# Kernel optimization log

Measured on AMD Instinct MI355X. Metric: run time of the kernel, lower is better.

## Reference

```python
import jax, jax.numpy as jnp
import numpy as np

B, T, DIM, HEADS, DH = 4, 2048, 1024, 16, 64  # dh = dim // heads


def setup_inputs() -> dict:
    key = jax.random.key(0)
    k1, k2, k3 = jax.random.split(key, 3)
    x = jax.random.normal(k1, (B, T, DIM), dtype=jnp.float32)
    # nn.Linear weights, stored as [in, out] for x @ W convention
    W_qkv = jax.random.normal(k2, (DIM, 3 * HEADS * DH), dtype=jnp.float32) * (DIM ** -0.5)
    W_o = jax.random.normal(k3, (HEADS * DH, DIM), dtype=jnp.float32) * ((HEADS * DH) ** -0.5)
    return {"x": x, "W_qkv": W_qkv, "W_o": W_o}


def reference(x, W_qkv, W_o):
    b, t, _ = x.shape
    qkv = x @ W_qkv  # [b, t, 3*h*dh]
    # einops 'b t (d k h) -> k b h t d' with k=3, h=HEADS: fused axis splits as (dh, 3, h)
    qkv = qkv.reshape(b, t, DH, 3, HEADS)
    qkv = jnp.transpose(qkv, (3, 0, 4, 1, 2))  # [3, b, h, t, dh]
    q, k, v = qkv[0], qkv[1], qkv[2]
    scale = DH ** -0.5
    scores = jnp.einsum('bhid,bhjd->bhij', q, k) * scale  # [b, h, t, t]
    attn = jax.nn.softmax(scores, axis=-1)
    out = jnp.einsum('bhij,bhjd->bhid', attn, v)  # [b, h, t, dh]
    out = jnp.transpose(out, (0, 2, 1, 3)).reshape(b, t, HEADS * DH)  # 'b h t d -> b t (h d)'
    return out @ W_o
```

## Files before the change

kernel.cpp:

```cpp
#include <hip/hip_runtime.h>

typedef __bf16 bf16;
typedef __bf16 bf16x2 __attribute__((ext_vector_type(2)));
typedef __bf16 bf16x4 __attribute__((ext_vector_type(4)));
typedef __bf16 bf16x8 __attribute__((ext_vector_type(8)));
typedef float  f32x4  __attribute__((ext_vector_type(4)));
typedef float  f32x16 __attribute__((ext_vector_type(16)));
typedef unsigned int u32;
typedef unsigned int u32x2 __attribute__((ext_vector_type(2)));
typedef unsigned int u32x4 __attribute__((ext_vector_type(4)));

#define LOG2E 1.44269504088896340736f
#define EXP_SC (0.125f * LOG2E)

#if __has_builtin(__builtin_amdgcn_exp2f)
#define EXP2F(x) __builtin_amdgcn_exp2f(x)
#else
#define EXP2F(x) __builtin_exp2f(x)
#endif

__device__ __forceinline__ u32 pk_bf16(float lo, float hi) {
  u32 a = __float_as_uint(lo) + 0x8000u;
  u32 b = __float_as_uint(hi) + 0x8000u;
  return __builtin_amdgcn_perm(b, a, 0x07060302);
}
#if __has_builtin(__builtin_amdgcn_cvt_pk_bf16_f32)
__device__ __forceinline__ u32 cvtpk(float lo, float hi) {
  bf16x2 t = __builtin_amdgcn_cvt_pk_bf16_f32(lo, hi);
  return __builtin_bit_cast(u32, t);
}
#else
__device__ __forceinline__ u32 cvtpk(float lo, float hi) { return pk_bf16(lo, hi); }
#endif
__device__ __forceinline__ unsigned short bf16r(float x) {
  return (unsigned short)((__float_as_uint(x) + 0x8000u) >> 16);
}

__device__ __forceinline__ f32x16 zero16() {
  f32x16 a;
#pragma unroll
  for (int i = 0; i < 16; i++) a[i] = 0.f;
  return a;
}

__device__ __forceinline__ void async_ld16(void* lds, const void* g) {
  __builtin_amdgcn_global_load_lds(
      (const __attribute__((address_space(1))) void*)(g),
      (__attribute__((address_space(3))) void*)(lds),
      16, 0, 0);
}

__global__ void prep_all(const float* __restrict__ x,    bf16* __restrict__ xb,
                         const float* __restrict__ Wqkv, bf16* __restrict__ wqkvT,
                         const float* __restrict__ Wo,   bf16* __restrict__ woT) {
  __shared__ float s[12288];
  const int bid = blockIdx.x;
  const int tid = threadIdx.x;
  if (bid < 8192) {
    int i = bid * 256 + tid;
    float4 v = ((const float4*)x)[i];
    u32x2 o = { pk_bf16(v.x, v.y), pk_bf16(v.z, v.w) };
    *(u32x2*)(xb + (size_t)i * 4) = o;
  } else if (bid < 8448) {
    const int k0 = (bid - 8192) * 4;
    for (int i = tid; i < 3072; i += 256) {
      int r = i / 768, c = (i - r * 768) * 4;
      *(float4*)(s + r * 3072 + c) = *(const float4*)(Wqkv + (size_t)(k0 + r) * 3072 + c);
    }
    __syncthreads();
    for (int n = tid; n < 3072; n += 256) {
      int dl = n & 63, h = (n >> 6) & 15, wch = n >> 10;
      int d = ((dl & 15) << 2) | (dl >> 4);
      int on = d * 48 + wch * 16 + h;
      u32x2 v = { pk_bf16(s[0 * 3072 + on], s[1 * 3072 + on]),
                  pk_bf16(s[2 * 3072 + on], s[3 * 3072 + on]) };
      *(u32x2*)(wqkvT + (size_t)n * 1024 + k0) = v;
    }
  } else {
    const int k0 = (bid - 8448) * 8;
    for (int i = tid; i < 2048; i += 256) {
      int r = i >> 8, c = (i & 255) * 4;
      *(float4*)(s + r * 1024 + c) = *(const float4*)(Wo + (size_t)(k0 + r) * 1024 + c);
    }
    __syncthreads();
    for (int n = tid; n < 1024; n += 256) {
      u32x4 v = { pk_bf16(s[0 * 1024 + n], s[1 * 1024 + n]),
                  pk_bf16(s[2 * 1024 + n], s[3 * 1024 + n]),
                  pk_bf16(s[4 * 1024 + n], s[5 * 1024 + n]),
                  pk_bf16(s[6 * 1024 + n], s[7 * 1024 + n]) };
      *(u32x4*)(woT + (size_t)n * 1024 + k0) = v;
    }
  }
}

template <int MODE>
__launch_bounds__(256, 2)
__global__ void gemm_bt(const bf16* __restrict__ A, const bf16* __restrict__ BT,
                        float* __restrict__ C, int N,
                        bf16* __restrict__ Qb, bf16* __restrict__ Kb, bf16* __restrict__ Vb) {
  constexpr int K = 1024;
  __shared__ bf16 sA[128 * 64];
  __shared__ bf16 sB[128 * 64];
  const int m0 = blockIdx.x * 128;
  const int n0 = blockIdx.y * 128;
  const int tid = threadIdx.x;
  const int lane = tid & 63;
  const int w = tid >> 6;
  const int wm = (w >> 1) * 64, wn = (w & 1) * 64;
  const int l15 = lane & 15, quad = lane >> 4;

  f32x4 acc[4][4];
  for (int i = 0; i < 4; i++)
    for (int j = 0; j < 4; j++) acc[i][j] = f32x4{0.f, 0.f, 0.f, 0.f};

  const int rT = tid >> 3;
  const int jT = (tid & 7) ^ (rT & 7);
  const bf16* gA = A  + (size_t)(m0 + rT) * K + jT * 8;
  const bf16* gB = BT + (size_t)(n0 + rT) * K + jT * 8;

  for (int k0 = 0; k0 < K; k0 += 64) {
    __syncthreads();
    for (int i = 0; i < 4; i++) {
      async_ld16((void*)(sA + (i * 256 + w * 64) * 8), gA + (size_t)i * 32 * K);
      async_ld16((void*)(sB + (i * 256 + w * 64) * 8), gB + (size_t)i * 32 * K);
    }
    gA += 64; gB += 64;
    __syncthreads();

    for (int kk = 0; kk < 2; kk++) {
      bf16x8 af[4], bfr[4];
      for (int ms = 0; ms < 4; ms++) {
        int r = wm + ms * 16 + l15;
        af[ms] = *(const bf16x8*)(sA + r * 64 + (((kk * 4 + quad) ^ (r & 7)) * 8));
      }
      for (int ns = 0; ns < 4; ns++) {
        int r = wn + ns * 16 + l15;
        bfr[ns] = *(const bf16x8*)(sB + r * 64 + (((kk * 4 + quad) ^ (r & 7)) * 8));
      }
      for (int ms = 0; ms < 4; ms++)
        for (int ns = 0; ns < 4; ns++)
          acc[ms][ns] = __builtin_amdgcn_mfma_f32_16x16x32_bf16(af[ms], bfr[ns], acc[ms][ns], 0, 0, 0);
    }
  }

  if (MODE == 0) {
    for (int ms = 0; ms < 4; ms++)
      for (int ns = 0; ns < 4; ns++)
        for (int r = 0; r < 4; r++) {
          int row = m0 + wm + ms * 16 + quad * 4 + r;
          int col = n0 + wn + ns * 16 + l15;
          C[(size_t)row * N + col] = acc[ms][ns][r];
        }
  } else {
    const int col0 = n0 + wn;
    const int wch = col0 >> 10;
    const int h = (col0 >> 6) & 15;
    if (wch != 2) {
      bf16* dst = (wch == 0) ? Qb : Kb;
      const float sc = (wch == 0) ? EXP_SC : 1.0f;
      for (int ms = 0; ms < 4; ms++)
        for (int r = 0; r < 4; r++) {
          int row = m0 + wm + ms * 16 + quad * 4 + r;
          int b = row >> 11, t = row & 2047;
          u32x2 v = { cvtpk(acc[ms][0][r] * sc, acc[ms][1][r] * sc),
                      cvtpk(acc[ms][2][r] * sc, acc[ms][3][r] * sc) };
          *(u32x2*)((unsigned short*)dst +
                    (((size_t)(b * 16 + h)) * 2048 + t) * 64 + l15 * 4) = v;
        }
    } else {
      for (int ms = 0; ms < 4; ms++)
        for (int ns = 0; ns < 4; ns++) {
          int row = m0 + wm + ms * 16 + quad * 4;
          int b = row >> 11, t = row & 2047;
          int d = l15 * 4 + ns;
          u32x2 v = { cvtpk(acc[ms][ns][0], acc[ms][ns][1]),
                      cvtpk(acc[ms][ns][2], acc[ms][ns][3]) };
          *(u32x2*)((unsigned short*)Vb +
                    (((size_t)(b * 16 + h)) * 64 + d) * 2048 + t) = v;
        }
    }
  }
}

__launch_bounds__(256, 3)
__global__ void attn_fwd(const bf16* __restrict__ Q, const bf16* __restrict__ K,
                         const bf16* __restrict__ VT, bf16* __restrict__ O) {
  __shared__ bf16 sK[64 * 64];
  __shared__ bf16 sV[4][64 * 64];
  const int bh = blockIdx.x;
  const int q0 = blockIdx.y * 128;
  const int tid = threadIdx.x;
  const int lane = tid & 63, w = tid >> 6;
  const int l31 = lane & 31, hi = lane >> 5;

  bf16x8 qf[4];
  {
    const bf16* qp = Q + ((size_t)bh * 2048 + q0 + w * 32 + l31) * 64 + hi * 8;
#pragma unroll
    for (int kq = 0; kq < 4; kq++) qf[kq] = *(const bf16x8*)(qp + kq * 16);
  }

  f32x16 oacc[2];
  oacc[0] = zero16(); oacc[1] = zero16();
  float rs = 0.f;

  const int cA = w * 128 + lane;
  const int rA = cA >> 3, jA = (cA & 7) ^ (rA & 7);
  const bf16* gK = K  + ((size_t)bh * 2048 + rA) * 64 + jA * 8;
  const bf16* gV = VT + ((size_t)bh * 64 + rA) * 2048 + jA * 8;

  int fo[2][4];
#pragma unroll
  for (int sub = 0; sub < 2; sub++)
#pragma unroll
    for (int st = 0; st < 4; st++) {
      int r = sub * 32 + l31;
      fo[sub][st] = r * 64 + (((st * 2 + hi) ^ (r & 7)) * 8);
    }

  async_ld16((void*)(sK + w * 1024),           gK);
  async_ld16((void*)(sK + w * 1024 + 512),     gK + 512);
  async_ld16((void*)(sV[0] + w * 1024),        gV);
  async_ld16((void*)(sV[0] + w * 1024 + 512),  gV + 16384);
  gK += 4096; gV += 64;

  auto expF = [&](f32x16 (&S)[2], bf16x8 (&F)[4]) {
#pragma unroll
    for (int ks = 0; ks < 2; ks++) {
      float p[16];
#pragma unroll
      for (int r = 0; r < 16; r++) p[r] = EXP2F(S[ks][r]);
      rs += (((p[0] + p[1]) + (p[2] + p[3])) + ((p[4] + p[5]) + (p[6] + p[7])))
          + (((p[8] + p[9]) + (p[10] + p[11])) + ((p[12] + p[13]) + (p[14] + p[15])));
      u32 c0 = cvtpk(p[0],  p[1]),  c1 = cvtpk(p[2],  p[3]);
      u32 c2 = cvtpk(p[4],  p[5]),  c3 = cvtpk(p[6],  p[7]);
      u32 c4 = cvtpk(p[8],  p[9]),  c5 = cvtpk(p[10], p[11]);
      u32 c6 = cvtpk(p[12], p[13]), c7 = cvtpk(p[14], p[15]);
      asm("v_permlane32_swap_b32 %0, %1" : "+v"(c0), "+v"(c2));
      asm("v_permlane32_swap_b32 %0, %1" : "+v"(c1), "+v"(c3));
      asm("v_permlane32_swap_b32 %0, %1" : "+v"(c4), "+v"(c6));
      asm("v_permlane32_swap_b32 %0, %1" : "+v"(c5), "+v"(c7));
      u32x4 f0 = { c0, c1, c2, c3 };
      u32x4 f1 = { c4, c5, c6, c7 };
      F[ks * 2 + 0] = __builtin_bit_cast(bf16x8, f0);
      F[ks * 2 + 1] = __builtin_bit_cast(bf16x8, f1);
    }
  };

  auto step = [&](int t, f32x16 (&Scur)[2], f32x16 (&Sprev)[2]) {
    __syncthreads();
    bf16x8 kf[2][4];
#pragma unroll
    for (int ks = 0; ks < 2; ks++)
#pragma unroll
      for (int kq = 0; kq < 4; kq++)
        kf[ks][kq] = *(const bf16x8*)(sK + fo[ks][kq]);
    __syncthreads();
    if (t < 31) {
      bf16* vn = (bf16*)sV[(t + 1) & 3];
      async_ld16((void*)(sK + w * 1024),          gK);
      async_ld16((void*)(sK + w * 1024 + 512),    gK + 512);
      async_ld16((void*)(vn + w * 1024),          gV);
      async_ld16((void*)(vn + w * 1024 + 512),    gV + 16384);
      gK += 4096; gV += 64;
    }
    __builtin_amdgcn_s_setprio(1);
#pragma unroll
    for (int ks = 0; ks < 2; ks++) {
      f32x16 a = zero16();
      a = __builtin_amdgcn_mfma_f32_32x32x16_bf16(kf[ks][0], qf[0], a, 0, 0, 0);
      a = __builtin_amdgcn_mfma_f32_32x32x16_bf16(kf[ks][1], qf[1], a, 0, 0, 0);
      a = __builtin_amdgcn_mfma_f32_32x32x16_bf16(kf[ks][2], qf[2], a, 0, 0, 0);
      a = __builtin_amdgcn_mfma_f32_32x32x16_bf16(kf[ks][3], qf[3], a, 0, 0, 0);
      Scur[ks] = a;
    }
    __builtin_amdgcn_s_setprio(0);
    const bf16* vb = sV[(t - 1) & 3];
    bf16x8 vf[2][4];
#pragma unroll
    for (int ds = 0; ds < 2; ds++)
#pragma unroll
      for (int kk = 0; kk < 4; kk++)
        vf[ds][kk] = *(const bf16x8*)(vb + fo[ds][kk]);
    bf16x8 F[4];
    expF(Sprev, F);
    __builtin_amdgcn_s_setprio(1);
#pragma unroll
    for (int ds = 0; ds < 2; ds++) {
      f32x16 a = oacc[ds];
      a = __builtin_amdgcn_mfma_f32_32x32x16_bf16(vf[ds][0], F[0], a, 0, 0, 0);
      a = __builtin_amdgcn_mfma_f32_32x32x16_bf16(vf[ds][1], F[1], a, 0, 0, 0);
      a = __builtin_amdgcn_mfma_f32_32x32x16_bf16(vf[ds][2], F[2], a, 0, 0, 0);
      a = __builtin_amdgcn_mfma_f32_32x32x16_bf16(vf[ds][3], F[3], a, 0, 0, 0);
      oacc[ds] = a;
    }
    __builtin_amdgcn_s_setprio(0);
  };

  f32x16 SA[2], SB[2];

  {
    __syncthreads();
    bf16x8 kf[2][4];
#pragma unroll
    for (int ks = 0; ks < 2; ks++)
#pragma unroll
      for (int kq = 0; kq < 4; kq++)
        kf[ks][kq] = *(const bf16x8*)(sK + fo[ks][kq]);
    __syncthreads();
    {
      bf16* vn = (bf16*)sV[1];
      async_ld16((void*)(sK + w * 1024),          gK);
      async_ld16((void*)(sK + w * 1024 + 512),    gK + 512);
      async_ld16((void*)(vn + w * 1024),          gV);
      async_ld16((void*)(vn + w * 1024 + 512),    gV + 16384);
      gK += 4096; gV += 64;
    }
    __builtin_amdgcn_s_setprio(1);
#pragma unroll
    for (int ks = 0; ks < 2; ks++) {
      f32x16 a = zero16();
      a = __builtin_amdgcn_mfma_f32_32x32x16_bf16(kf[ks][0], qf[0], a, 0, 0, 0);
      a = __builtin_amdgcn_mfma_f32_32x32x16_bf16(kf[ks][1], qf[1], a, 0, 0, 0);
      a = __builtin_amdgcn_mfma_f32_32x32x16_bf16(kf[ks][2], qf[2], a, 0, 0, 0);
      a = __builtin_amdgcn_mfma_f32_32x32x16_bf16(kf[ks][3], qf[3], a, 0, 0, 0);
      SA[ks] = a;
    }
    __builtin_amdgcn_s_setprio(0);
  }

  for (int t = 1; t < 31; t += 2) {
    step(t,     SB, SA);
    step(t + 1, SA, SB);
  }
  step(31, SB, SA);

  {
    const bf16* vb = sV[31 & 3];
    bf16x8 vf[2][4];
#pragma unroll
    for (int ds = 0; ds < 2; ds++)
#pragma unroll
      for (int kk = 0; kk < 4; kk++)
        vf[ds][kk] = *(const bf16x8*)(vb + fo[ds][kk]);
    bf16x8 F[4];
    expF(SB, F);
#pragma unroll
    for (int ds = 0; ds < 2; ds++) {
      f32x16 a = oacc[ds];
      a = __builtin_amdgcn_mfma_f32_32x32x16_bf16(vf[ds][0], F[0], a, 0, 0, 0);
      a = __builtin_amdgcn_mfma_f32_32x32x16_bf16(vf[ds][1], F[1], a, 0, 0, 0);
      a = __builtin_amdgcn_mfma_f32_32x32x16_bf16(vf[ds][2], F[2], a, 0, 0, 0);
      a = __builtin_amdgcn_mfma_f32_32x32x16_bf16(vf[ds][3], F[3], a, 0, 0, 0);
      oacc[ds] = a;
    }
  }

  float rt = rs + __shfl_xor(rs, 32, 64);
  float inv = 1.0f / rt;
  const int b = bh >> 4, h = bh & 15;
  const int trow = q0 + w * 32 + l31;
#pragma unroll
  for (int ds = 0; ds < 2; ds++)
#pragma unroll
    for (int g = 0; g < 4; g++) {
      int d = ds * 32 + g * 8 + hi * 4;
      u32x2 pkv = { cvtpk(oacc[ds][g * 4 + 0] * inv, oacc[ds][g * 4 + 1] * inv),
                    cvtpk(oacc[ds][g * 4 + 2] * inv, oacc[ds][g * 4 + 3] * inv) };
      *(u32x2*)(O + ((size_t)b * 2048 + trow) * 1024 + h * 64 + d) = pkv;
    }
}

extern "C" void kernel_launch(void* const* d_in, const int* in_sizes, int n_in,
                              void* d_out, int out_size, void* d_ws, size_t ws_size,
                              hipStream_t stream) {
  const float* x    = (const float*)d_in[0];
  const float* Wqkv = (const float*)d_in[1];
  const float* Wo   = (const float*)d_in[2];
  float* out = (float*)d_out;
  char* ws = (char*)d_ws;

  bf16* wqkvT = (bf16*)(ws);
  bf16* woT   = (bf16*)(ws + 6291456);
  bf16* xb    = (bf16*)(ws + 8388608);
  bf16* Qb    = (bf16*)(ws + 25165824);
  bf16* Kb    = (bf16*)(ws + 41943040);
  bf16* VTb   = (bf16*)(ws + 58720256);
  bf16* AOb   = xb;

  prep_all<<<8576, 256, 0, stream>>>(x, xb, Wqkv, wqkvT, Wo, woT);
  gemm_bt<1><<<dim3(64, 24), 256, 0, stream>>>(xb, wqkvT, nullptr, 3072, Qb, Kb, VTb);
  attn_fwd<<<dim3(64, 16), 256, 0, stream>>>(Qb, Kb, VTb, AOb);
  gemm_bt<0><<<dim3(64, 8), 256, 0, stream>>>(AOb, woT, out, 1024, nullptr, nullptr, nullptr);
}
```

Baseline: 313.6 us.

## Double-buffer LDS tiles in GEMM and attention to drop a barrier per iteration

The projection GEMM now keeps two shared-memory tiles and prefetches the next K-slice while computing on the current one, removing the second __syncthreads per step. The attention kernel double-buffers the K tile as well, fuses the QK and PV MFMA phases into one loop body with a single barrier, and computes the softmax exp right after the scores. This targets load latency and barrier stalls, at the cost of extra LDS (which may limit occupancy) and less exp/MFMA interleaving across iterations.

```diff
diff --git a/kernel.cpp b/kernel.cpp
--- a/kernel.cpp
+++ b/kernel.cpp
@@ -99,8 +99,8 @@
                         float* __restrict__ C, int N,
                         bf16* __restrict__ Qb, bf16* __restrict__ Kb, bf16* __restrict__ Vb) {
   constexpr int K = 1024;
-  __shared__ bf16 sA[128 * 64];
-  __shared__ bf16 sB[128 * 64];
+  __shared__ bf16 sA[2][128 * 64];
+  __shared__ bf16 sB[2][128 * 64];
   const int m0 = blockIdx.x * 128;
   const int n0 = blockIdx.y * 128;
   const int tid = threadIdx.x;
@@ -118,29 +118,41 @@
   const bf16* gA = A  + (size_t)(m0 + rT) * K + jT * 8;
   const bf16* gB = BT + (size_t)(n0 + rT) * K + jT * 8;
 
+  for (int i = 0; i < 4; i++) {
+    async_ld16((void*)(sA[0] + (i * 256 + w * 64) * 8), gA + (size_t)i * 32 * K);
+    async_ld16((void*)(sB[0] + (i * 256 + w * 64) * 8), gB + (size_t)i * 32 * K);
+  }
+  gA += 64; gB += 64;
+
+  int cur = 0;
   for (int k0 = 0; k0 < K; k0 += 64) {
     __syncthreads();
-    for (int i = 0; i < 4; i++) {
-      async_ld16((void*)(sA + (i * 256 + w * 64) * 8), gA + (size_t)i * 32 * K);
-      async_ld16((void*)(sB + (i * 256 + w * 64) * 8), gB + (size_t)i * 32 * K);
-    }
-    gA += 64; gB += 64;
-    __syncthreads();
-
+    const bf16* a = sA[cur];
+    const bf16* b = sB[cur];
+    if (k0 + 64 < K) {
+      bf16* na = sA[cur ^ 1];
+      bf16* nb = sB[cur ^ 1];
+      for (int i = 0; i < 4; i++) {
+        async_ld16((void*)(na + (i * 256 + w * 64) * 8), gA + (size_t)i * 32 * K);
+        async_ld16((void*)(nb + (i * 256 + w * 64) * 8), gB + (size_t)i * 32 * K);
+      }
+      gA += 64; gB += 64;
+    }
     for (int kk = 0; kk < 2; kk++) {
       bf16x8 af[4], bfr[4];
       for (int ms = 0; ms < 4; ms++) {
         int r = wm + ms * 16 + l15;
-        af[ms] = *(const bf16x8*)(sA + r * 64 + (((kk * 4 + quad) ^ (r & 7)) * 8));
+        af[ms] = *(const bf16x8*)(a + r * 64 + (((kk * 4 + quad) ^ (r & 7)) * 8));
       }
       for (int ns = 0; ns < 4; ns++) {
         int r = wn + ns * 16 + l15;
-        bfr[ns] = *(const bf16x8*)(sB + r * 64 + (((kk * 4 + quad) ^ (r & 7)) * 8));
+        bfr[ns] = *(const bf16x8*)(b + r * 64 + (((kk * 4 + quad) ^ (r & 7)) * 8));
       }
       for (int ms = 0; ms < 4; ms++)
         for (int ns = 0; ns < 4; ns++)
           acc[ms][ns] = __builtin_amdgcn_mfma_f32_16x16x32_bf16(af[ms], bfr[ns], acc[ms][ns], 0, 0, 0);
     }
+    cur ^= 1;
   }
 
   if (MODE == 0) {
@@ -185,7 +197,7 @@
 __launch_bounds__(256, 3)
 __global__ void attn_fwd(const bf16* __restrict__ Q, const bf16* __restrict__ K,
                          const bf16* __restrict__ VT, bf16* __restrict__ O) {
-  __shared__ bf16 sK[64 * 64];
+  __shared__ bf16 sK[2][64 * 64];
   __shared__ bf16 sV[4][64 * 64];
   const int bh = blockIdx.x;
   const int q0 = blockIdx.y * 128;
@@ -218,11 +230,13 @@
       fo[sub][st] = r * 64 + (((st * 2 + hi) ^ (r & 7)) * 8);
     }
 
-  async_ld16((void*)(sK + w * 1024),           gK);
-  async_ld16((void*)(sK + w * 1024 + 512),     gK + 512);
-  async_ld16((void*)(sV[0] + w * 1024),        gV);
-  async_ld16((void*)(sV[0] + w * 1024 + 512),  gV + 16384);
-  gK += 4096; gV += 64;
+  auto stage = [&](bf16* kb, bf16* vb) {
+    async_ld16((void*)(kb + w * 1024),        gK);
+    async_ld16((void*)(kb + w * 1024 + 512),  gK + 512);
+    async_ld16((void*)(vb + w * 1024),        gV);
+    async_ld16((void*)(vb + w * 1024 + 512),  gV + 16384);
+    gK += 4096; gV += 64;
+  };
 
   auto expF = [&](f32x16 (&S)[2], bf16x8 (&F)[4]) {
 #pragma unroll
@@ -247,23 +261,20 @@
     }
   };
 
-  auto step = [&](int t, f32x16 (&Scur)[2], f32x16 (&Sprev)[2]) {
-    __syncthreads();
+  stage(sK[0], sV[0]);
+
+  f32x16 S[2];
+  bf16x8 F[4];
+
+  {
+    __syncthreads();
+    stage(sK[1], sV[1]);
     bf16x8 kf[2][4];
 #pragma unroll
     for (int ks = 0; ks < 2; ks++)
 #pragma unroll
       for (int kq = 0; kq < 4; kq++)
-        kf[ks][kq] = *(const bf16x8*)(sK + fo[ks][kq]);
-    __syncthreads();
-    if (t < 31) {
-      bf16* vn = (bf16*)sV[(t + 1) & 3];
-      async_ld16((void*)(sK + w * 1024),          gK);
-      async_ld16((void*)(sK + w * 1024 + 512),    gK + 512);
-      async_ld16((void*)(vn + w * 1024),          gV);
-      async_ld16((void*)(vn + w * 1024 + 512),    gV + 16384);
-      gK += 4096; gV += 64;
-    }
+        kf[ks][kq] = *(const bf16x8*)(sK[0] + fo[ks][kq]);
     __builtin_amdgcn_s_setprio(1);
 #pragma unroll
     for (int ks = 0; ks < 2; ks++) {
@@ -272,19 +283,39 @@
       a = __builtin_amdgcn_mfma_f32_32x32x16_bf16(kf[ks][1], qf[1], a, 0, 0, 0);
       a = __builtin_amdgcn_mfma_f32_32x32x16_bf16(kf[ks][2], qf[2], a, 0, 0, 0);
       a = __builtin_amdgcn_mfma_f32_32x32x16_bf16(kf[ks][3], qf[3], a, 0, 0, 0);
-      Scur[ks] = a;
+      S[ks] = a;
     }
     __builtin_amdgcn_s_setprio(0);
+    expF(S, F);
+  }
+
+  for (int t = 1; t < 32; ++t) {
+    __syncthreads();
+    if (t < 31) stage(sK[(t + 1) & 1], sV[(t + 1) & 3]);
+    const bf16* kb = sK[t & 1];
     const bf16* vb = sV[(t - 1) & 3];
+    bf16x8 kf[2][4];
+#pragma unroll
+    for (int ks = 0; ks < 2; ks++)
+#pragma unroll
+      for (int kq = 0; kq < 4; kq++)
+        kf[ks][kq] = *(const bf16x8*)(kb + fo[ks][kq]);
     bf16x8 vf[2][4];
 #pragma unroll
     for (int ds = 0; ds < 2; ds++)
 #pragma unroll
       for (int kk = 0; kk < 4; kk++)
         vf[ds][kk] = *(const bf16x8*)(vb + fo[ds][kk]);
-    bf16x8 F[4];
-    expF(Sprev, F);
     __builtin_amdgcn_s_setprio(1);
+#pragma unroll
+    for (int ks = 0; ks < 2; ks++) {
+      f32x16 a = zero16();
+      a = __builtin_amdgcn_mfma_f32_32x32x16_bf16(kf[ks][0], qf[0], a, 0, 0, 0);
+      a = __builtin_amdgcn_mfma_f32_32x32x16_bf16(kf[ks][1], qf[1], a, 0, 0, 0);
+      a = __builtin_amdgcn_mfma_f32_32x32x16_bf16(kf[ks][2], qf[2], a, 0, 0, 0);
+      a = __builtin_amdgcn_mfma_f32_32x32x16_bf16(kf[ks][3], qf[3], a, 0, 0, 0);
+      S[ks] = a;
+    }
 #pragma unroll
     for (int ds = 0; ds < 2; ds++) {
       f32x16 a = oacc[ds];
@@ -295,56 +326,17 @@
       oacc[ds] = a;
     }
     __builtin_amdgcn_s_setprio(0);
-  };
-
-  f32x16 SA[2], SB[2];
+    expF(S, F);
+  }
 
   {
-    __syncthreads();
-    bf16x8 kf[2][4];
-#pragma unroll
-    for (int ks = 0; ks < 2; ks++)
-#pragma unroll
-      for (int kq = 0; kq < 4; kq++)
-        kf[ks][kq] = *(const bf16x8*)(sK + fo[ks][kq]);
-    __syncthreads();
-    {
-      bf16* vn = (bf16*)sV[1];
-      async_ld16((void*)(sK + w * 1024),          gK);
-      async_ld16((void*)(sK + w * 1024 + 512),    gK + 512);
-      async_ld16((void*)(vn + w * 1024),          gV);
-      async_ld16((void*)(vn + w * 1024 + 512),    gV + 16384);
-      gK += 4096; gV += 64;
-    }
-    __builtin_amdgcn_s_setprio(1);
-#pragma unroll
-    for (int ks = 0; ks < 2; ks++) {
-      f32x16 a = zero16();
-      a = __builtin_amdgcn_mfma_f32_32x32x16_bf16(kf[ks][0], qf[0], a, 0, 0, 0);
-      a = __builtin_amdgcn_mfma_f32_32x32x16_bf16(kf[ks][1], qf[1], a, 0, 0, 0);
-      a = __builtin_amdgcn_mfma_f32_32x32x16_bf16(kf[ks][2], qf[2], a, 0, 0, 0);
-      a = __builtin_amdgcn_mfma_f32_32x32x16_bf16(kf[ks][3], qf[3], a, 0, 0, 0);
-      SA[ks] = a;
-    }
-    __builtin_amdgcn_s_setprio(0);
-  }
-
-  for (int t = 1; t < 31; t += 2) {
-    step(t,     SB, SA);
-    step(t + 1, SA, SB);
-  }
-  step(31, SB, SA);
-
-  {
-    const bf16* vb = sV[31 & 3];
+    const bf16* vb = sV[3];
     bf16x8 vf[2][4];
 #pragma unroll
     for (int ds = 0; ds < 2; ds++)
 #pragma unroll
       for (int kk = 0; kk < 4; kk++)
         vf[ds][kk] = *(const bf16x8*)(vb + fo[ds][kk]);
-    bf16x8 F[4];
-    expF(SB, F);
 #pragma unroll
     for (int ds = 0; ds < 2; ds++) {
       f32x16 a = oacc[ds];
```

Result: faster. 291.3 us (-7.1%).

## Process two query blocks per attention workgroup to reuse K/V tiles

Applied to the files above, without the earlier changes.

Each attention workgroup now handles 256 query rows as two 128-row sub-blocks that share each staged K and V tile. The grid shrinks to half as many blocks, and launch bounds drop from 3 to 2 waves per SIMD to make room for the doubled accumulators. This halves K/V global and LDS traffic per query. It also removes the software pipeline that overlapped the exp of the previous tile with the current QK MFMA; the second sub-block's work now has to provide that overlap instead. Fewer resident blocks and the loss of that explicit overlap are the risks.

```diff
diff --git a/kernel.cpp b/kernel.cpp
--- a/kernel.cpp
+++ b/kernel.cpp
@@ -182,27 +182,29 @@
   }
 }
 
-__launch_bounds__(256, 3)
+__launch_bounds__(256, 2)
 __global__ void attn_fwd(const bf16* __restrict__ Q, const bf16* __restrict__ K,
                          const bf16* __restrict__ VT, bf16* __restrict__ O) {
   __shared__ bf16 sK[64 * 64];
   __shared__ bf16 sV[4][64 * 64];
   const int bh = blockIdx.x;
-  const int q0 = blockIdx.y * 128;
+  const int q0 = blockIdx.y * 256;
   const int tid = threadIdx.x;
   const int lane = tid & 63, w = tid >> 6;
   const int l31 = lane & 31, hi = lane >> 5;
 
-  bf16x8 qf[4];
-  {
-    const bf16* qp = Q + ((size_t)bh * 2048 + q0 + w * 32 + l31) * 64 + hi * 8;
-#pragma unroll
-    for (int kq = 0; kq < 4; kq++) qf[kq] = *(const bf16x8*)(qp + kq * 16);
-  }
-
-  f32x16 oacc[2];
-  oacc[0] = zero16(); oacc[1] = zero16();
-  float rs = 0.f;
+  bf16x8 qf[2][4];
+#pragma unroll
+  for (int qb = 0; qb < 2; qb++) {
+    const bf16* qp = Q + ((size_t)bh * 2048 + q0 + qb * 128 + w * 32 + l31) * 64 + hi * 8;
+#pragma unroll
+    for (int kq = 0; kq < 4; kq++) qf[qb][kq] = *(const bf16x8*)(qp + kq * 16);
+  }
+
+  f32x16 oacc[2][2];
+  oacc[0][0] = zero16(); oacc[0][1] = zero16();
+  oacc[1][0] = zero16(); oacc[1][1] = zero16();
+  float rs[2] = {0.f, 0.f};
 
   const int cA = w * 128 + lane;
   const int rA = cA >> 3, jA = (cA & 7) ^ (rA & 7);
@@ -218,20 +220,22 @@
       fo[sub][st] = r * 64 + (((st * 2 + hi) ^ (r & 7)) * 8);
     }
 
-  async_ld16((void*)(sK + w * 1024),           gK);
-  async_ld16((void*)(sK + w * 1024 + 512),     gK + 512);
-  async_ld16((void*)(sV[0] + w * 1024),        gV);
-  async_ld16((void*)(sV[0] + w * 1024 + 512),  gV + 16384);
-  gK += 4096; gV += 64;
-
-  auto expF = [&](f32x16 (&S)[2], bf16x8 (&F)[4]) {
+  auto stage = [&](bf16* vb) {
+    async_ld16((void*)(sK + w * 1024),        gK);
+    async_ld16((void*)(sK + w * 1024 + 512),  gK + 512);
+    async_ld16((void*)(vb + w * 1024),        gV);
+    async_ld16((void*)(vb + w * 1024 + 512),  gV + 16384);
+    gK += 4096; gV += 64;
+  };
+
+  auto expF = [&](f32x16 (&S)[2], bf16x8 (&F)[4], float& rsv) {
 #pragma unroll
     for (int ks = 0; ks < 2; ks++) {
       float p[16];
 #pragma unroll
       for (int r = 0; r < 16; r++) p[r] = EXP2F(S[ks][r]);
-      rs += (((p[0] + p[1]) + (p[2] + p[3])) + ((p[4] + p[5]) + (p[6] + p[7])))
-          + (((p[8] + p[9]) + (p[10] + p[11])) + ((p[12] + p[13]) + (p[14] + p[15])));
+      rsv += (((p[0] + p[1]) + (p[2] + p[3])) + ((p[4] + p[5]) + (p[6] + p[7])))
+           + (((p[8] + p[9]) + (p[10] + p[11])) + ((p[12] + p[13]) + (p[14] + p[15])));
       u32 c0 = cvtpk(p[0],  p[1]),  c1 = cvtpk(p[2],  p[3]);
       u32 c2 = cvtpk(p[4],  p[5]),  c3 = cvtpk(p[6],  p[7]);
       u32 c4 = cvtpk(p[8],  p[9]),  c5 = cvtpk(p[10], p[11]);
@@ -247,7 +251,9 @@
     }
   };
 
-  auto step = [&](int t, f32x16 (&Scur)[2], f32x16 (&Sprev)[2]) {
+  stage((bf16*)sV[0]);
+
+  for (int t = 0; t < 32; ++t) {
     __syncthreads();
     bf16x8 kf[2][4];
 #pragma unroll
@@ -256,119 +262,85 @@
       for (int kq = 0; kq < 4; kq++)
         kf[ks][kq] = *(const bf16x8*)(sK + fo[ks][kq]);
     __syncthreads();
-    if (t < 31) {
-      bf16* vn = (bf16*)sV[(t + 1) & 3];
-      async_ld16((void*)(sK + w * 1024),          gK);
-      async_ld16((void*)(sK + w * 1024 + 512),    gK + 512);
-      async_ld16((void*)(vn + w * 1024),          gV);
-      async_ld16((void*)(vn + w * 1024 + 512),    gV + 16384);
-      gK += 4096; gV += 64;
-    }
+    if (t < 31) stage((bf16*)sV[(t + 1) & 3]);
+    const bf16* vb = sV[t & 3];
+
+    f32x16 S0[2], S1[2];
     __builtin_amdgcn_s_setprio(1);
 #pragma unroll
     for (int ks = 0; ks < 2; ks++) {
       f32x16 a = zero16();
-      a = __builtin_amdgcn_mfma_f32_32x32x16_bf16(kf[ks][0], qf[0], a, 0, 0, 0);
-      a = __builtin_amdgcn_mfma_f32_32x32x16_bf16(kf[ks][1], qf[1], a, 0, 0, 0);
-      a = __builtin_amdgcn_mfma_f32_32x32x16_bf16(kf[ks][2], qf[2], a, 0, 0, 0);
-      a = __builtin_amdgcn_mfma_f32_32x32x16_bf16(kf[ks][3], qf[3], a, 0, 0, 0);
-      Scur[ks] = a;
+      a = __builtin_amdgcn_mfma_f32_32x32x16_bf16(kf[ks][0], qf[0][0], a, 0, 0, 0);
+      a = __builtin_amdgcn_mfma_f32_32x32x16_bf16(kf[ks][1], qf[0][1], a, 0, 0, 0);
+      a = __builtin_amdgcn_mfma_f32_32x32x16_bf16(kf[ks][2], qf[0][2], a, 0, 0, 0);
+      a = __builtin_amdgcn_mfma_f32_32x32x16_bf16(kf[ks][3], qf[0][3], a, 0, 0, 0);
+      S0[ks] = a;
+    }
+#pragma unroll
+    for (int ks = 0; ks < 2; ks++) {
+      f32x16 a = zero16();
+      a = __builtin_amdgcn_mfma_f32_32x32x16_bf16(kf[ks][0], qf[1][0], a, 0, 0, 0);
+      a = __builtin_amdgcn_mfma_f32_32x32x16_bf16(kf[ks][1], qf[1][1], a, 0, 0, 0);
+      a = __builtin_amdgcn_mfma_f32_32x32x16_bf16(kf[ks][2], qf[1][2], a, 0, 0, 0);
+      a = __builtin_amdgcn_mfma_f32_32x32x16_bf16(kf[ks][3], qf[1][3], a, 0, 0, 0);
+      S1[ks] = a;
     }
     __builtin_amdgcn_s_setprio(0);
-    const bf16* vb = sV[(t - 1) & 3];
+
+    bf16x8 F[4];
+    expF(S0, F, rs[0]);
+
     bf16x8 vf[2][4];
 #pragma unroll
     for (int ds = 0; ds < 2; ds++)
 #pragma unroll
       for (int kk = 0; kk < 4; kk++)
         vf[ds][kk] = *(const bf16x8*)(vb + fo[ds][kk]);
-    bf16x8 F[4];
-    expF(Sprev, F);
+
     __builtin_amdgcn_s_setprio(1);
 #pragma unroll
     for (int ds = 0; ds < 2; ds++) {
-      f32x16 a = oacc[ds];
+      f32x16 a = oacc[0][ds];
       a = __builtin_amdgcn_mfma_f32_32x32x16_bf16(vf[ds][0], F[0], a, 0, 0, 0);
       a = __builtin_amdgcn_mfma_f32_32x32x16_bf16(vf[ds][1], F[1], a, 0, 0, 0);
       a = __builtin_amdgcn_mfma_f32_32x32x16_bf16(vf[ds][2], F[2], a, 0, 0, 0);
       a = __builtin_amdgcn_mfma_f32_32x32x16_bf16(vf[ds][3], F[3], a, 0, 0, 0);
-      oacc[ds] = a;
+      oacc[0][ds] = a;
     }
     __builtin_amdgcn_s_setprio(0);
-  };
-
-  f32x16 SA[2], SB[2];
-
-  {
-    __syncthreads();
-    bf16x8 kf[2][4];
-#pragma unroll
-    for (int ks = 0; ks < 2; ks++)
-#pragma unroll
-      for (int kq = 0; kq < 4; kq++)
-        kf[ks][kq] = *(const bf16x8*)(sK + fo[ks][kq]);
-    __syncthreads();
-    {
-      bf16* vn = (bf16*)sV[1];
-      async_ld16((void*)(sK + w * 1024),          gK);
-      async_ld16((void*)(sK + w * 1024 + 512),    gK + 512);
-      async_ld16((void*)(vn + w * 1024),          gV);
-      async_ld16((void*)(vn + w * 1024 + 512),    gV + 16384);
-      gK += 4096; gV += 64;
-    }
+
+    bf16x8 G[4];
+    expF(S1, G, rs[1]);
+
     __builtin_amdgcn_s_setprio(1);
 #pragma unroll
-    for (int ks = 0; ks < 2; ks++) {
-      f32x16 a = zero16();
-      a = __builtin_amdgcn_mfma_f32_32x32x16_bf16(kf[ks][0], qf[0], a, 0, 0, 0);
-      a = __builtin_amdgcn_mfma_f32_32x32x16_bf16(kf[ks][1], qf[1], a, 0, 0, 0);
-      a = __builtin_amdgcn_mfma_f32_32x32x16_bf16(kf[ks][2], qf[2], a, 0, 0, 0);
-      a = __builtin_amdgcn_mfma_f32_32x32x16_bf16(kf[ks][3], qf[3], a, 0, 0, 0);
-      SA[ks] = a;
+    for (int ds = 0; ds < 2; ds++) {
+      f32x16 a = oacc[1][ds];
+      a = __builtin_amdgcn_mfma_f32_32x32x16_bf16(vf[ds][0], G[0], a, 0, 0, 0);
+      a = __builtin_amdgcn_mfma_f32_32x32x16_bf16(vf[ds][1], G[1], a, 0, 0, 0);
+      a = __builtin_amdgcn_mfma_f32_32x32x16_bf16(vf[ds][2], G[2], a, 0, 0, 0);
+      a = __builtin_amdgcn_mfma_f32_32x32x16_bf16(vf[ds][3], G[3], a, 0, 0, 0);
+      oacc[1][ds] = a;
     }
     __builtin_amdgcn_s_setprio(0);
   }
 
-  for (int t = 1; t < 31; t += 2) {
-    step(t,     SB, SA);
-    step(t + 1, SA, SB);
-  }
-  step(31, SB, SA);
-
-  {
-    const bf16* vb = sV[31 & 3];
-    bf16x8 vf[2][4];
+  const int b = bh >> 4, h = bh & 15;
+#pragma unroll
+  for (int qb = 0; qb < 2; qb++) {
+    float rt = rs[qb] + __shfl_xor(rs[qb], 32, 64);
+    float inv = 1.0f / rt;
+    const int trow = q0 + qb * 128 + w * 32 + l31;
 #pragma unroll
     for (int ds = 0; ds < 2; ds++)
 #pragma unroll
-      for (int kk = 0; kk < 4; kk++)
-        vf[ds][kk] = *(const bf16x8*)(vb + fo[ds][kk]);
-    bf16x8 F[4];
-    expF(SB, F);
-#pragma unroll
-    for (int ds = 0; ds < 2; ds++) {
-      f32x16 a = oacc[ds];
-      a = __builtin_amdgcn_mfma_f32_32x32x16_bf16(vf[ds][0], F[0], a, 0, 0, 0);
-      a = __builtin_amdgcn_mfma_f32_32x32x16_bf16(vf[ds][1], F[1], a, 0, 0, 0);
-      a = __builtin_amdgcn_mfma_f32_32x32x16_bf16(vf[ds][2], F[2], a, 0, 0, 0);
-      a = __builtin_amdgcn_mfma_f32_32x32x16_bf16(vf[ds][3], F[3], a, 0, 0, 0);
-      oacc[ds] = a;
-    }
-  }
-
-  float rt = rs + __shfl_xor(rs, 32, 64);
-  float inv = 1.0f / rt;
-  const int b = bh >> 4, h = bh & 15;
-  const int trow = q0 + w * 32 + l31;
-#pragma unroll
-  for (int ds = 0; ds < 2; ds++)
-#pragma unroll
-    for (int g = 0; g < 4; g++) {
-      int d = ds * 32 + g * 8 + hi * 4;
-      u32x2 pkv = { cvtpk(oacc[ds][g * 4 + 0] * inv, oacc[ds][g * 4 + 1] * inv),
-                    cvtpk(oacc[ds][g * 4 + 2] * inv, oacc[ds][g * 4 + 3] * inv) };
-      *(u32x2*)(O + ((size_t)b * 2048 + trow) * 1024 + h * 64 + d) = pkv;
-    }
+      for (int g = 0; g < 4; g++) {
+        int d = ds * 32 + g * 8 + hi * 4;
+        u32x2 pkv = { cvtpk(oacc[qb][ds][g * 4 + 0] * inv, oacc[qb][ds][g * 4 + 1] * inv),
+                      cvtpk(oacc[qb][ds][g * 4 + 2] * inv, oacc[qb][ds][g * 4 + 3] * inv) };
+        *(u32x2*)(O + ((size_t)b * 2048 + trow) * 1024 + h * 64 + d) = pkv;
+      }
+  }
 }
 
 extern "C" void kernel_launch(void* const* d_in, const int* in_sizes, int n_in,
@@ -390,6 +362,6 @@
 
   prep_all<<<8576, 256, 0, stream>>>(x, xb, Wqkv, wqkvT, Wo, woT);
   gemm_bt<1><<<dim3(64, 24), 256, 0, stream>>>(xb, wqkvT, nullptr, 3072, Qb, Kb, VTb);
-  attn_fwd<<<dim3(64, 16), 256, 0, stream>>>(Qb, Kb, VTb, AOb);
+  attn_fwd<<<dim3(64, 8), 256, 0, stream>>>(Qb, Kb, VTb, AOb);
   gemm_bt<0><<<dim3(64, 8), 256, 0, stream>>>(AOb, woT, out, 1024, nullptr, nullptr, nullptr);
 }
```

Measured after the change: 260.3 us. 17.0% less time.
